# Kernel optimization log

Hardware: AMD Instinct MI355X
Metric: run time of the kernel (lower is better)

The kernel has to match this reference:

```python
import jax, jax.numpy as jnp
import numpy as np

B, T, D, H = 2048, 512, 32, 64


def _gru_layer(x, W_ih, W_hh, b_ih, b_hh):
    # x: [B, T, Din]; W_ih: [3H, Din]; W_hh: [3H, H]; gate order r, z, n (PyTorch).
    xp = jnp.einsum('btd,gd->btg', x, W_ih) + b_ih  # precompute input projections [B,T,3H]

    def step(h, xt):
        gh = h @ W_hh.T + b_hh                      # [B,3H]
        ir, iz, inn = jnp.split(xt, 3, axis=-1)
        hr, hz, hn = jnp.split(gh, 3, axis=-1)
        r = jax.nn.sigmoid(ir + hr)
        z = jax.nn.sigmoid(iz + hz)
        n = jnp.tanh(inn + r * hn)
        h_new = (1.0 - z) * n + z * h
        return h_new, h_new

    h0 = jnp.zeros((x.shape[0], W_hh.shape[1]), dtype=x.dtype)
    _, ys = jax.lax.scan(step, h0, xp.transpose(1, 0, 2))  # ys: [T,B,H]
    return ys.transpose(1, 0, 2)                           # [B,T,H]


def setup_inputs() -> dict:
    key = jax.random.key(0)
    ks = jax.random.split(key, 12)
    s_in = 1.0 / np.sqrt(H)
    u = lambda k, shp: jax.random.uniform(k, shp, jnp.float32, -s_in, s_in)
    return {
        'x': jax.random.normal(ks[0], (B, T, D), jnp.float32),
        'W_ih0': u(ks[1], (3 * H, D)),  'W_hh0': u(ks[2], (3 * H, H)),
        'b_ih0': u(ks[3], (3 * H,)),    'b_hh0': u(ks[4], (3 * H,)),
        'W_ih1': u(ks[5], (3 * H, H)),  'W_hh1': u(ks[6], (3 * H, H)),
        'b_ih1': u(ks[7], (3 * H,)),    'b_hh1': u(ks[8], (3 * H,)),
        'fc_w': u(ks[9], (1, H)),       'fc_b': u(ks[10], (1,)),
    }


def reference(x, W_ih0, W_hh0, b_ih0, b_hh0, W_ih1, W_hh1, b_ih1, b_hh1, fc_w, fc_b):
    # 2-layer GRU (eval mode: inter-layer dropout is identity) + linear head on last step.
    h1 = _gru_layer(x, W_ih0, W_hh0, b_ih0, b_hh0)   # [B,T,H]
    h2 = _gru_layer(h1, W_ih1, W_hh1, b_ih1, b_hh1)  # [B,T,H]
    out = h2[:, -1, :] @ fc_w.T + fc_b               # [B,1]
    return out[:, 0]                                  # [B]
```

## Files before the change

kernel.cpp:

```cpp
#include <hip/hip_runtime.h>

#define Bsz  2048
#define Tlen 512
#define Din  32
#define Hd   64
#define BT   16
#define HS   72
#define SLOT (BT * HS)
#define SPINB (1 << 14)

typedef _Float16 half8 __attribute__((ext_vector_type(8)));
typedef _Float16 half4 __attribute__((ext_vector_type(4)));
typedef float    f32x4 __attribute__((ext_vector_type(4)));

#define MFMA(a, b, c) __builtin_amdgcn_mfma_f32_16x16x32_f16((a), (b), (c), 0, 0, 0)

__device__ __forceinline__ half8 load8s(const float* p, float s) {
    half8 r;
#pragma unroll
    for (int j = 0; j < 8; ++j) r[j] = (_Float16)(p[j] * s);
    return r;
}
__device__ __forceinline__ half8 cvt8(float4 a, float4 b) {
    half8 r;
    r[0] = (_Float16)a.x; r[1] = (_Float16)a.y; r[2] = (_Float16)a.z; r[3] = (_Float16)a.w;
    r[4] = (_Float16)b.x; r[5] = (_Float16)b.y; r[6] = (_Float16)b.z; r[7] = (_Float16)b.w;
    return r;
}

__device__ __forceinline__ half4 gate_upd(const f32x4& gr, const f32x4& gz,
                                          const f32x4& anx, const f32x4& anh,
                                          float hst[4]) {
    half4 pk;
#pragma unroll
    for (int r = 0; r < 4; ++r) {
        float Er = __builtin_amdgcn_exp2f(gr[r]);
        float rr = __builtin_amdgcn_rcpf(1.0f + Er);
        float yy = anx[r] + rr * anh[r];
        float En = __builtin_amdgcn_exp2f(yy);
        float Ez = __builtin_amdgcn_exp2f(gz[r]);
        float num = Ez * (1.0f - En) + hst[r] * (1.0f + En);
        float den = (1.0f + Ez) * (1.0f + En);
        hst[r] = num * __builtin_amdgcn_rcpf(den);
        pk[r] = (_Float16)hst[r];
    }
    return pk;
}

#define SPIN_GE(CTR, TGT, CACHE)                                         \
  do {                                                                   \
    if ((CACHE) < (TGT)) {                                               \
      int v_ = (CACHE);                                                  \
      for (int sp_ = 0; v_ < (TGT) && sp_ < SPINB; ++sp_) {              \
        if (lane == 0)                                                   \
          v_ = __hip_atomic_load(&CTR, __ATOMIC_ACQUIRE,                 \
                                 __HIP_MEMORY_SCOPE_WORKGROUP);          \
        v_ = __builtin_amdgcn_readfirstlane(v_);                         \
        if (v_ < (TGT)) __builtin_amdgcn_s_sleep(1);                     \
      }                                                                  \
      (CACHE) = v_;                                                      \
    }                                                                    \
    __builtin_amdgcn_sched_barrier(0);                                   \
  } while (0)

__global__ __launch_bounds__(512, 2)
void gru_fused(const float* __restrict__ x,
               const float* __restrict__ Wih0, const float* __restrict__ Whh0,
               const float* __restrict__ bih0, const float* __restrict__ bhh0,
               const float* __restrict__ Wih1, const float* __restrict__ Whh1,
               const float* __restrict__ bih1, const float* __restrict__ bhh1,
               const float* __restrict__ fcw,  const float* __restrict__ fcb,
               float* __restrict__ out)
{
    __shared__ _Float16 h1r[4 * SLOT];
    __shared__ _Float16 h2r[2 * SLOT];
    __shared__ float hfin[BT][Hd];
    __shared__ int c1, c2, u1;

    const int tid  = threadIdx.x;
    const int lane = tid & 63;
    const int wave = tid >> 6;
    const int grp  = wave >> 2;
    const int wg   = wave & 3;
    const int m    = lane & 15;
    const int quad = lane >> 4;
    const int col  = (wg << 4) + m;
    const int gc   = (wg << 4) + (quad << 2);
    const int b0   = blockIdx.x << 4;

    for (int idx = tid; idx < SLOT; idx += 512) {
        h1r[3 * SLOT + idx] = (_Float16)0.f;
        h2r[SLOT + idx]     = (_Float16)0.f;
    }
    if (tid == 0) { c1 = 0; c2 = 0; u1 = 0; }

    const float sRZ = -1.44269504f;
    const float sN  = -2.88539008f;
    const int rdoff = m * HS + quad * 8;
    const int wroff = m * HS + gc;
    float hst[4] = {0.f, 0.f, 0.f, 0.f};

    __syncthreads();

    if (grp == 0) {
        half8 wx0, wx1, wx2, wh[2][3];
        f32x4 brz0v, brz1v, binv, bhnv;
        wx0 = load8s(Wih0 + (      col) * Din + quad * 8, sRZ);
        wx1 = load8s(Wih0 + ( 64 + col) * Din + quad * 8, sRZ);
        wx2 = load8s(Wih0 + (128 + col) * Din + quad * 8, sN);
#pragma unroll
        for (int kb = 0; kb < 2; ++kb) {
            wh[kb][0] = load8s(Whh0 + (      col) * Hd + kb * 32 + quad * 8, sRZ);
            wh[kb][1] = load8s(Whh0 + ( 64 + col) * Hd + kb * 32 + quad * 8, sRZ);
            wh[kb][2] = load8s(Whh0 + (128 + col) * Hd + kb * 32 + quad * 8, sN);
        }
#pragma unroll
        for (int r = 0; r < 4; ++r) {
            brz0v[r] = sRZ * (bih0[gc + r] + bhh0[gc + r]);
            brz1v[r] = sRZ * (bih0[64 + gc + r] + bhh0[64 + gc + r]);
            binv[r]  = sN * bih0[128 + gc + r];
            bhnv[r]  = sN * bhh0[128 + gc + r];
        }
        const float* xgp = x + (size_t)(b0 + m) * (Tlen * Din) + quad * 8;
        float4 x0a, x0b, x1a, x1b;
        x0a = *(const float4*)(xgp);        x0b = *(const float4*)(xgp + 4);
        x1a = *(const float4*)(xgp + Din);  x1b = *(const float4*)(xgp + Din + 4);
        int c1v = 0, u1v = 0;

#define STEP_A(T, xa_, xb_)                                              \
  do {                                                                   \
    SPIN_GE(c1, 4 * (T), c1v);                \
    const _Float16* s1 = h1r + (((T) + 3) & 3) * SLOT + rdoff;           \
    half8 bh0 = *(const half8*)s1;                                       \
    half8 bh1 = *(const half8*)(s1 + 32);                                \
    half8 ax = cvt8(xa_, xb_);                                           \
    { const int nx = ((T) + 2 < Tlen) ? (T) + 2 : Tlen - 1;              \
      const float* p = xgp + (size_t)nx * Din;                           \
      xa_ = *(const float4*)p; xb_ = *(const float4*)(p + 4); }          \
    f32x4 arx = brz0v, azx = brz1v, anx = binv;                          \
    f32x4 arh = {0.f,0.f,0.f,0.f}, azh = {0.f,0.f,0.f,0.f}, anh = bhnv;  \
    arh = MFMA(wh[0][0], bh0, arh); arh = MFMA(wh[1][0], bh1, arh);      \
    azh = MFMA(wh[0][1], bh0, azh); azh = MFMA(wh[1][1], bh1, azh);      \
    anh = MFMA(wh[0][2], bh0, anh); anh = MFMA(wh[1][2], bh1, anh);      \
    arx = MFMA(wx0, ax, arx);                                            \
    azx = MFMA(wx1, ax, azx);                                            \
    anx = MFMA(wx2, ax, anx);                                            \
    f32x4 gr = arx + arh, gz = azx + azh;                                \
    half4 pk = gate_upd(gr, gz, anx, anh, hst);                          \
    SPIN_GE(u1, 4 * ((T) - 3), u1v);          \
    *(half4*)(h1r + ((T) & 3) * SLOT + wroff) = pk;                      \
    asm volatile("s_waitcnt lgkmcnt(0)" ::: "memory");                   \
    if (lane == 0)                                                       \
      __hip_atomic_fetch_add(&c1, 1, __ATOMIC_RELEASE,                   \
                             __HIP_MEMORY_SCOPE_WORKGROUP);              \
  } while (0)

        for (int t = 0; t < Tlen; t += 2) {
            STEP_A(t,     x0a, x0b);
            STEP_A(t + 1, x1a, x1b);
        }
#undef STEP_A
    } else {
        half8 wx[2][3], wh[2][3];
        f32x4 brz0v, brz1v, binv, bhnv;
#pragma unroll
        for (int kb = 0; kb < 2; ++kb) {
            wx[kb][0] = load8s(Wih1 + (      col) * Hd + kb * 32 + quad * 8, sRZ);
            wx[kb][1] = load8s(Wih1 + ( 64 + col) * Hd + kb * 32 + quad * 8, sRZ);
            wx[kb][2] = load8s(Wih1 + (128 + col) * Hd + kb * 32 + quad * 8, sN);
            wh[kb][0] = load8s(Whh1 + (      col) * Hd + kb * 32 + quad * 8, sRZ);
            wh[kb][1] = load8s(Whh1 + ( 64 + col) * Hd + kb * 32 + quad * 8, sRZ);
            wh[kb][2] = load8s(Whh1 + (128 + col) * Hd + kb * 32 + quad * 8, sN);
        }
#pragma unroll
        for (int r = 0; r < 4; ++r) {
            brz0v[r] = sRZ * (bih1[gc + r] + bhh1[gc + r]);
            brz1v[r] = sRZ * (bih1[64 + gc + r] + bhh1[64 + gc + r]);
            binv[r]  = sN * bih1[128 + gc + r];
            bhnv[r]  = sN * bhh1[128 + gc + r];
        }
        int c1v = 0, c2v = 0;

#define STEP_B(T)                                                        \
  do {                                                                   \
    SPIN_GE(c2, 4 * (T), c2v);                \
    SPIN_GE(c1, 4 * ((T) + 1), c1v);          \
    const _Float16* s1 = h1r + ((T) & 3) * SLOT + rdoff;    \
    const _Float16* s2 = h2r + (((T) + 1) & 1) * SLOT + rdoff;  \
    half8 bx0 = *(const half8*)s1;                                       \
    half8 bx1 = *(const half8*)(s1 + 32);                                \
    half8 bh0 = *(const half8*)s2;                                       \
    half8 bh1 = *(const half8*)(s2 + 32);                                \
    f32x4 arx = brz0v, azx = brz1v, anx = binv;                          \
    f32x4 arh = {0.f,0.f,0.f,0.f}, azh = {0.f,0.f,0.f,0.f}, anh = bhnv;  \
    arx = MFMA(wx[0][0], bx0, arx); arx = MFMA(wx[1][0], bx1, arx);      \
    azx = MFMA(wx[0][1], bx0, azx); azx = MFMA(wx[1][1], bx1, azx);      \
    anx = MFMA(wx[0][2], bx0, anx); anx = MFMA(wx[1][2], bx1, anx);      \
    arh = MFMA(wh[0][0], bh0, arh); arh = MFMA(wh[1][0], bh1, arh);      \
    azh = MFMA(wh[0][1], bh0, azh); azh = MFMA(wh[1][1], bh1, azh);      \
    anh = MFMA(wh[0][2], bh0, anh); anh = MFMA(wh[1][2], bh1, anh);      \
    asm volatile("s_waitcnt lgkmcnt(0)" ::: "memory");   \
    if (lane == 0)                                                       \
      __hip_atomic_fetch_add(&u1, 1, __ATOMIC_RELEASE,                   \
                             __HIP_MEMORY_SCOPE_WORKGROUP);              \
    f32x4 gr = arx + arh, gz = azx + azh;                                \
    half4 pk = gate_upd(gr, gz, anx, anh, hst);                          \
    *(half4*)(h2r + ((T) & 1) * SLOT + wroff) = pk;                      \
    if ((T) == Tlen - 1) {                                               \
      f32x4 fv;                                                          \
      for (int r = 0; r < 4; ++r) fv[r] = hst[r];                        \
      *(f32x4*)(&hfin[m][gc]) = fv;                                      \
    }                                                                    \
    asm volatile("s_waitcnt lgkmcnt(0)" ::: "memory");                   \
    if (lane == 0)                                                       \
      __hip_atomic_fetch_add(&c2, 1, __ATOMIC_RELEASE,                   \
                             __HIP_MEMORY_SCOPE_WORKGROUP);              \
  } while (0)

        for (int t = 0; t < Tlen; t += 2) {
            STEP_B(t);
            STEP_B(t + 1);
        }
#undef STEP_B

        if (wg == 0) {
            SPIN_GE(c2, 4 * Tlen, c2v);
            if (lane < BT) {
                float acc = fcb[0];
                for (int c = 0; c < Hd; ++c) acc += hfin[lane][c] * fcw[c];
                out[b0 + lane] = acc;
            }
        }
    }
}

extern "C" void kernel_launch(void* const* d_in, const int* in_sizes, int n_in,
                              void* d_out, int out_size, void* d_ws, size_t ws_size,
                              hipStream_t stream) {
    gru_fused<<<dim3(Bsz / BT), dim3(512), 0, stream>>>(
        (const float*)d_in[0],
        (const float*)d_in[1], (const float*)d_in[2],
        (const float*)d_in[3], (const float*)d_in[4],
        (const float*)d_in[5], (const float*)d_in[6],
        (const float*)d_in[7], (const float*)d_in[8],
        (const float*)d_in[9], (const float*)d_in[10],
        (float*)d_out);
}
```

Baseline: 535.8 us.

## Replace LDS spin-counter sync with lockstep barrier regions between GRU layers

Removes the atomic counter spin-wait protocol between the layer-0 and layer-1 wave groups. Both groups now advance in lockstep regions separated by s_barrier, with layer 1 running one step behind layer 0. Layer 0's input projection for the next step is computed in the second half of each region so it overlaps the layer-1 gate update. This trades spin-polling and sleep latency for two full-workgroup barriers per step, drops the 2-blocks-per-CU launch bound, and uses a larger LDS arena.

```diff
diff --git a/kernel.cpp b/kernel.cpp
--- a/kernel.cpp
+++ b/kernel.cpp
@@ -6,14 +6,19 @@
 #define Hd   64
 #define BT   16
 #define HS   72
-#define SLOT (BT * HS)
-#define SPINB (1 << 14)
+#define BUFE 2048
 
 typedef _Float16 half8 __attribute__((ext_vector_type(8)));
 typedef _Float16 half4 __attribute__((ext_vector_type(4)));
 typedef float    f32x4 __attribute__((ext_vector_type(4)));
 
 #define MFMA(a, b, c) __builtin_amdgcn_mfma_f32_16x16x32_f16((a), (b), (c), 0, 0, 0)
+
+#define BARRIER()                                              \
+  do {                                                         \
+    asm volatile("s_waitcnt lgkmcnt(0)" ::: "memory");         \
+    __builtin_amdgcn_s_barrier();                              \
+  } while (0)
 
 __device__ __forceinline__ half8 load8s(const float* p, float s) {
     half8 r;
@@ -47,23 +52,7 @@
     return pk;
 }
 
-#define SPIN_GE(CTR, TGT, CACHE)                                         \
-  do {                                                                   \
-    if ((CACHE) < (TGT)) {                                               \
-      int v_ = (CACHE);                                                  \
-      for (int sp_ = 0; v_ < (TGT) && sp_ < SPINB; ++sp_) {              \
-        if (lane == 0)                                                   \
-          v_ = __hip_atomic_load(&CTR, __ATOMIC_ACQUIRE,                 \
-                                 __HIP_MEMORY_SCOPE_WORKGROUP);          \
-        v_ = __builtin_amdgcn_readfirstlane(v_);                         \
-        if (v_ < (TGT)) __builtin_amdgcn_s_sleep(1);                     \
-      }                                                                  \
-      (CACHE) = v_;                                                      \
-    }                                                                    \
-    __builtin_amdgcn_sched_barrier(0);                                   \
-  } while (0)
-
-__global__ __launch_bounds__(512, 2)
+__global__ __launch_bounds__(512)
 void gru_fused(const float* __restrict__ x,
                const float* __restrict__ Wih0, const float* __restrict__ Whh0,
                const float* __restrict__ bih0, const float* __restrict__ bhh0,
@@ -72,10 +61,8 @@
                const float* __restrict__ fcw,  const float* __restrict__ fcb,
                float* __restrict__ out)
 {
-    __shared__ _Float16 h1r[4 * SLOT];
-    __shared__ _Float16 h2r[2 * SLOT];
+    __shared__ _Float16 arena[4 * BUFE];
     __shared__ float hfin[BT][Hd];
-    __shared__ int c1, c2, u1;
 
     const int tid  = threadIdx.x;
     const int lane = tid & 63;
@@ -88,11 +75,7 @@
     const int gc   = (wg << 4) + (quad << 2);
     const int b0   = blockIdx.x << 4;
 
-    for (int idx = tid; idx < SLOT; idx += 512) {
-        h1r[3 * SLOT + idx] = (_Float16)0.f;
-        h2r[SLOT + idx]     = (_Float16)0.f;
-    }
-    if (tid == 0) { c1 = 0; c2 = 0; u1 = 0; }
+    for (int idx = tid; idx < 4 * BUFE; idx += 512) arena[idx] = (_Float16)0.f;
 
     const float sRZ = -1.44269504f;
     const float sN  = -2.88539008f;
@@ -100,14 +83,12 @@
     const int wroff = m * HS + gc;
     float hst[4] = {0.f, 0.f, 0.f, 0.f};
 
-    __syncthreads();
-
+    half8 wx[2][3], wh[2][3];
+    f32x4 brz0v, brz1v, binv, bhnv;
     if (grp == 0) {
-        half8 wx0, wx1, wx2, wh[2][3];
-        f32x4 brz0v, brz1v, binv, bhnv;
-        wx0 = load8s(Wih0 + (      col) * Din + quad * 8, sRZ);
-        wx1 = load8s(Wih0 + ( 64 + col) * Din + quad * 8, sRZ);
-        wx2 = load8s(Wih0 + (128 + col) * Din + quad * 8, sN);
+        wx[0][0] = load8s(Wih0 + (      col) * Din + quad * 8, sRZ);
+        wx[0][1] = load8s(Wih0 + ( 64 + col) * Din + quad * 8, sRZ);
+        wx[0][2] = load8s(Wih0 + (128 + col) * Din + quad * 8, sN);
 #pragma unroll
         for (int kb = 0; kb < 2; ++kb) {
             wh[kb][0] = load8s(Whh0 + (      col) * Hd + kb * 32 + quad * 8, sRZ);
@@ -121,48 +102,7 @@
             binv[r]  = sN * bih0[128 + gc + r];
             bhnv[r]  = sN * bhh0[128 + gc + r];
         }
-        const float* xgp = x + (size_t)(b0 + m) * (Tlen * Din) + quad * 8;
-        float4 x0a, x0b, x1a, x1b;
-        x0a = *(const float4*)(xgp);        x0b = *(const float4*)(xgp + 4);
-        x1a = *(const float4*)(xgp + Din);  x1b = *(const float4*)(xgp + Din + 4);
-        int c1v = 0, u1v = 0;
-
-#define STEP_A(T, xa_, xb_)                                              \
-  do {                                                                   \
-    SPIN_GE(c1, 4 * (T), c1v);                \
-    const _Float16* s1 = h1r + (((T) + 3) & 3) * SLOT + rdoff;           \
-    half8 bh0 = *(const half8*)s1;                                       \
-    half8 bh1 = *(const half8*)(s1 + 32);                                \
-    half8 ax = cvt8(xa_, xb_);                                           \
-    { const int nx = ((T) + 2 < Tlen) ? (T) + 2 : Tlen - 1;              \
-      const float* p = xgp + (size_t)nx * Din;                           \
-      xa_ = *(const float4*)p; xb_ = *(const float4*)(p + 4); }          \
-    f32x4 arx = brz0v, azx = brz1v, anx = binv;                          \
-    f32x4 arh = {0.f,0.f,0.f,0.f}, azh = {0.f,0.f,0.f,0.f}, anh = bhnv;  \
-    arh = MFMA(wh[0][0], bh0, arh); arh = MFMA(wh[1][0], bh1, arh);      \
-    azh = MFMA(wh[0][1], bh0, azh); azh = MFMA(wh[1][1], bh1, azh);      \
-    anh = MFMA(wh[0][2], bh0, anh); anh = MFMA(wh[1][2], bh1, anh);      \
-    arx = MFMA(wx0, ax, arx);                                            \
-    azx = MFMA(wx1, ax, azx);                                            \
-    anx = MFMA(wx2, ax, anx);                                            \
-    f32x4 gr = arx + arh, gz = azx + azh;                                \
-    half4 pk = gate_upd(gr, gz, anx, anh, hst);                          \
-    SPIN_GE(u1, 4 * ((T) - 3), u1v);          \
-    *(half4*)(h1r + ((T) & 3) * SLOT + wroff) = pk;                      \
-    asm volatile("s_waitcnt lgkmcnt(0)" ::: "memory");                   \
-    if (lane == 0)                                                       \
-      __hip_atomic_fetch_add(&c1, 1, __ATOMIC_RELEASE,                   \
-                             __HIP_MEMORY_SCOPE_WORKGROUP);              \
-  } while (0)
-
-        for (int t = 0; t < Tlen; t += 2) {
-            STEP_A(t,     x0a, x0b);
-            STEP_A(t + 1, x1a, x1b);
-        }
-#undef STEP_A
     } else {
-        half8 wx[2][3], wh[2][3];
-        f32x4 brz0v, brz1v, binv, bhnv;
 #pragma unroll
         for (int kb = 0; kb < 2; ++kb) {
             wx[kb][0] = load8s(Wih1 + (      col) * Hd + kb * 32 + quad * 8, sRZ);
@@ -179,58 +119,112 @@
             binv[r]  = sN * bih1[128 + gc + r];
             bhnv[r]  = sN * bhh1[128 + gc + r];
         }
-        int c1v = 0, c2v = 0;
-
-#define STEP_B(T)                                                        \
+    }
+
+    const float* xgp = x + (size_t)(b0 + m) * (Tlen * Din) + quad * 8;
+    float4 x0a, x0b, x1a, x1b;
+    f32x4 xar, xaz, xan;
+    if (grp == 0) {
+        x0a = *(const float4*)(xgp);        x0b = *(const float4*)(xgp + 4);
+        x1a = *(const float4*)(xgp + Din);  x1b = *(const float4*)(xgp + Din + 4);
+        half8 ax = cvt8(x0a, x0b);
+        xar = brz0v; xar = MFMA(wx[0][0], ax, xar);
+        xaz = brz1v; xaz = MFMA(wx[0][1], ax, xaz);
+        xan = binv;  xan = MFMA(wx[0][2], ax, xan);
+        {
+            const float* p = xgp + 2 * Din;
+            x0a = *(const float4*)p; x0b = *(const float4*)(p + 4);
+        }
+    }
+    half8 bx0, bx1;
+    f32x4 arx, azx, anx, arh, azh, anh;
+
+    __syncthreads();
+
+#define REGION(I, RO, WO, XA, XB, DO1)                                   \
   do {                                                                   \
-    SPIN_GE(c2, 4 * (T), c2v);                \
-    SPIN_GE(c1, 4 * ((T) + 1), c1v);          \
-    const _Float16* s1 = h1r + ((T) & 3) * SLOT + rdoff;    \
-    const _Float16* s2 = h2r + (((T) + 1) & 1) * SLOT + rdoff;  \
-    half8 bx0 = *(const half8*)s1;                                       \
-    half8 bx1 = *(const half8*)(s1 + 32);                                \
-    half8 bh0 = *(const half8*)s2;                                       \
-    half8 bh1 = *(const half8*)(s2 + 32);                                \
-    f32x4 arx = brz0v, azx = brz1v, anx = binv;                          \
-    f32x4 arh = {0.f,0.f,0.f,0.f}, azh = {0.f,0.f,0.f,0.f}, anh = bhnv;  \
-    arx = MFMA(wx[0][0], bx0, arx); arx = MFMA(wx[1][0], bx1, arx);      \
-    azx = MFMA(wx[0][1], bx0, azx); azx = MFMA(wx[1][1], bx1, azx);      \
-    anx = MFMA(wx[0][2], bx0, anx); anx = MFMA(wx[1][2], bx1, anx);      \
-    arh = MFMA(wh[0][0], bh0, arh); arh = MFMA(wh[1][0], bh1, arh);      \
-    azh = MFMA(wh[0][1], bh0, azh); azh = MFMA(wh[1][1], bh1, azh);      \
-    anh = MFMA(wh[0][2], bh0, anh); anh = MFMA(wh[1][2], bh1, anh);      \
-    asm volatile("s_waitcnt lgkmcnt(0)" ::: "memory");   \
-    if (lane == 0)                                                       \
-      __hip_atomic_fetch_add(&u1, 1, __ATOMIC_RELEASE,                   \
-                             __HIP_MEMORY_SCOPE_WORKGROUP);              \
-    f32x4 gr = arx + arh, gz = azx + azh;                                \
-    half4 pk = gate_upd(gr, gz, anx, anh, hst);                          \
-    *(half4*)(h2r + ((T) & 1) * SLOT + wroff) = pk;                      \
-    if ((T) == Tlen - 1) {                                               \
-      f32x4 fv;                                                          \
-      for (int r = 0; r < 4; ++r) fv[r] = hst[r];                        \
-      *(f32x4*)(&hfin[m][gc]) = fv;                                      \
+                             \
+    if (grp == 0) {                                                      \
+      const _Float16* s1 = arena + (RO) + rdoff;                         \
+      half8 bh0 = *(const half8*)s1;                                     \
+      half8 bh1 = *(const half8*)(s1 + 32);                              \
+      f32x4 arh0 = {0.f,0.f,0.f,0.f}, azh0 = {0.f,0.f,0.f,0.f};          \
+      f32x4 anh0 = bhnv;                                                 \
+      arh0 = MFMA(wh[0][0], bh0, arh0); arh0 = MFMA(wh[1][0], bh1, arh0);\
+      azh0 = MFMA(wh[0][1], bh0, azh0); azh0 = MFMA(wh[1][1], bh1, azh0);\
+      anh0 = MFMA(wh[0][2], bh0, anh0); anh0 = MFMA(wh[1][2], bh1, anh0);\
+      f32x4 gr = xar + arh0, gz = xaz + azh0;                            \
+      half4 pk = gate_upd(gr, gz, xan, anh0, hst);                       \
+      *(half4*)(arena + (WO) + wroff) = pk;                              \
+    } else if (DO1) {                                                    \
+      const _Float16* s2 = arena + 2 * BUFE + (RO) + rdoff;              \
+      half8 bh0 = *(const half8*)s2;                                     \
+      half8 bh1 = *(const half8*)(s2 + 32);                              \
+      arx = brz0v; azx = brz1v; anx = binv;                              \
+      arh = (f32x4){0.f,0.f,0.f,0.f}; azh = (f32x4){0.f,0.f,0.f,0.f};    \
+      anh = bhnv;                                                        \
+      arx = MFMA(wx[0][0], bx0, arx); arx = MFMA(wx[1][0], bx1, arx);    \
+      azx = MFMA(wx[0][1], bx0, azx); azx = MFMA(wx[1][1], bx1, azx);    \
+      anx = MFMA(wx[0][2], bx0, anx); anx = MFMA(wx[1][2], bx1, anx);    \
+      arh = MFMA(wh[0][0], bh0, arh); arh = MFMA(wh[1][0], bh1, arh);    \
+      azh = MFMA(wh[0][1], bh0, azh); azh = MFMA(wh[1][1], bh1, azh);    \
+      anh = MFMA(wh[0][2], bh0, anh); anh = MFMA(wh[1][2], bh1, anh);    \
     }                                                                    \
-    asm volatile("s_waitcnt lgkmcnt(0)" ::: "memory");                   \
-    if (lane == 0)                                                       \
-      __hip_atomic_fetch_add(&c2, 1, __ATOMIC_RELEASE,                   \
-                             __HIP_MEMORY_SCOPE_WORKGROUP);              \
+    BARRIER();                                                           \
+                             \
+    if (grp == 0) {                                                      \
+      half8 ax = cvt8(XA, XB);                               \
+      { const int nx = ((I) + 3 < Tlen) ? (I) + 3 : Tlen - 1;            \
+        const float* p = xgp + (size_t)nx * Din;                         \
+        XA = *(const float4*)p; XB = *(const float4*)(p + 4); }          \
+      xar = brz0v; xar = MFMA(wx[0][0], ax, xar);                        \
+      xaz = brz1v; xaz = MFMA(wx[0][1], ax, xaz);                        \
+      xan = binv;  xan = MFMA(wx[0][2], ax, xan);                        \
+    } else {                                                             \
+      if (DO1) {                                                         \
+        f32x4 gr = arx + arh, gz = azx + azh;                            \
+        half4 pk = gate_upd(gr, gz, anx, anh, hst);                      \
+        *(half4*)(arena + 2 * BUFE + (WO) + wroff) = pk;                 \
+      }                                                                  \
+      const _Float16* s1n = arena + (WO) + rdoff;     \
+      bx0 = *(const half8*)s1n;                                          \
+      bx1 = *(const half8*)(s1n + 32);                                   \
+    }                                                                    \
+    BARRIER();                                                           \
   } while (0)
 
-        for (int t = 0; t < Tlen; t += 2) {
-            STEP_B(t);
-            STEP_B(t + 1);
-        }
-#undef STEP_B
-
-        if (wg == 0) {
-            SPIN_GE(c2, 4 * Tlen, c2v);
-            if (lane < BT) {
-                float acc = fcb[0];
-                for (int c = 0; c < Hd; ++c) acc += hfin[lane][c] * fcw[c];
-                out[b0 + lane] = acc;
-            }
-        }
+    REGION(0, BUFE, 0, x1a, x1b, 0);
+    for (int i = 1; i + 1 < Tlen; i += 2) {
+        REGION(i,     0,    BUFE, x0a, x0b, 1);
+        REGION(i + 1, BUFE, 0,    x1a, x1b, 1);
+    }
+    REGION(Tlen - 1, 0, BUFE, x0a, x0b, 1);
+#undef REGION
+
+    if (grp == 1) {
+        const _Float16* s2 = arena + 2 * BUFE + BUFE + rdoff;
+        half8 bh0 = *(const half8*)s2;
+        half8 bh1 = *(const half8*)(s2 + 32);
+        f32x4 arx2 = brz0v, azx2 = brz1v, anx2 = binv;
+        f32x4 arh2 = {0.f,0.f,0.f,0.f}, azh2 = {0.f,0.f,0.f,0.f}, anh2 = bhnv;
+        arx2 = MFMA(wx[0][0], bx0, arx2); arx2 = MFMA(wx[1][0], bx1, arx2);
+        azx2 = MFMA(wx[0][1], bx0, azx2); azx2 = MFMA(wx[1][1], bx1, azx2);
+        anx2 = MFMA(wx[0][2], bx0, anx2); anx2 = MFMA(wx[1][2], bx1, anx2);
+        arh2 = MFMA(wh[0][0], bh0, arh2); arh2 = MFMA(wh[1][0], bh1, arh2);
+        azh2 = MFMA(wh[0][1], bh0, azh2); azh2 = MFMA(wh[1][1], bh1, azh2);
+        anh2 = MFMA(wh[0][2], bh0, anh2); anh2 = MFMA(wh[1][2], bh1, anh2);
+        f32x4 gr = arx2 + arh2, gz = azx2 + azh2;
+        gate_upd(gr, gz, anx2, anh2, hst);
+        f32x4 fv;
+#pragma unroll
+        for (int r = 0; r < 4; ++r) fv[r] = hst[r];
+        *(f32x4*)(&hfin[m][gc]) = fv;
+    }
+    __syncthreads();
+    if (tid < BT) {
+        float acc = fcb[0];
+        for (int c = 0; c < Hd; ++c) acc += hfin[tid][c] * fcw[c];
+        out[b0 + tid] = acc;
     }
 }
 
```

New measurement: 487.6 us. -9.0%, faster.

## Collapse each GRU layer to a single wave with deeper inter-layer ring

Applied to the files above, without the earlier changes.

Each layer's recurrence is now computed by one wave covering all 64 hidden columns, where before four waves each handled 16 columns. This removes intra-layer cross-wave synchronisation on every timestep. The layer-1 to layer-2 buffer grows to an 8-slot ring so layer 1 can run further ahead, and the FC head becomes a register dot product with shuffles. The trade-off is 4x more serial MFMA and gate work per wave per step, much higher register pressure from holding all weights, and only 128 threads per block.

```diff
diff --git a/kernel.cpp b/kernel.cpp
--- a/kernel.cpp
+++ b/kernel.cpp
@@ -7,7 +7,8 @@
 #define BT   16
 #define HS   72
 #define SLOT (BT * HS)
-#define SPINB (1 << 14)
+#define RS   8
+#define SPINB 4096
 
 typedef _Float16 half8 __attribute__((ext_vector_type(8)));
 typedef _Float16 half4 __attribute__((ext_vector_type(4)));
@@ -28,9 +29,9 @@
     return r;
 }
 
-__device__ __forceinline__ half4 gate_upd(const f32x4& gr, const f32x4& gz,
-                                          const f32x4& anx, const f32x4& anh,
-                                          float hst[4]) {
+__device__ __forceinline__ half4 gate4(const f32x4& gr, const f32x4& gz,
+                                       const f32x4& anx, const f32x4& anh,
+                                       float* hst) {
     half4 pk;
 #pragma unroll
     for (int r = 0; r < 4; ++r) {
@@ -63,181 +64,192 @@
     __builtin_amdgcn_sched_barrier(0);                                   \
   } while (0)
 
-__global__ __launch_bounds__(512, 2)
-void gru_fused(const float* __restrict__ x,
-               const float* __restrict__ Wih0, const float* __restrict__ Whh0,
-               const float* __restrict__ bih0, const float* __restrict__ bhh0,
-               const float* __restrict__ Wih1, const float* __restrict__ Whh1,
-               const float* __restrict__ bih1, const float* __restrict__ bhh1,
-               const float* __restrict__ fcw,  const float* __restrict__ fcb,
-               float* __restrict__ out)
+__global__ __launch_bounds__(128, 1)
+void gru_ws(const float* __restrict__ x,
+            const float* __restrict__ Wih0, const float* __restrict__ Whh0,
+            const float* __restrict__ bih0, const float* __restrict__ bhh0,
+            const float* __restrict__ Wih1, const float* __restrict__ Whh1,
+            const float* __restrict__ bih1, const float* __restrict__ bhh1,
+            const float* __restrict__ fcw,  const float* __restrict__ fcb,
+            float* __restrict__ out)
 {
-    __shared__ _Float16 h1r[4 * SLOT];
+    __shared__ _Float16 ring[RS * SLOT];
     __shared__ _Float16 h2r[2 * SLOT];
-    __shared__ float hfin[BT][Hd];
-    __shared__ int c1, c2, u1;
+    __shared__ int c1, u1;
 
     const int tid  = threadIdx.x;
     const int lane = tid & 63;
-    const int wave = tid >> 6;
-    const int grp  = wave >> 2;
-    const int wg   = wave & 3;
+    const int wv   = tid >> 6;
+    const int q    = lane >> 4;
     const int m    = lane & 15;
-    const int quad = lane >> 4;
-    const int col  = (wg << 4) + m;
-    const int gc   = (wg << 4) + (quad << 2);
     const int b0   = blockIdx.x << 4;
 
-    for (int idx = tid; idx < SLOT; idx += 512) {
-        h1r[3 * SLOT + idx] = (_Float16)0.f;
-        h2r[SLOT + idx]     = (_Float16)0.f;
+    for (int idx = tid; idx < SLOT; idx += 128) {
+        ring[(RS - 1) * SLOT + idx] = (_Float16)0.f;
+        h2r[SLOT + idx]             = (_Float16)0.f;
     }
-    if (tid == 0) { c1 = 0; c2 = 0; u1 = 0; }
+    if (tid == 0) { c1 = 0; u1 = 0; }
 
     const float sRZ = -1.44269504f;
     const float sN  = -2.88539008f;
-    const int rdoff = m * HS + quad * 8;
-    const int wroff = m * HS + gc;
-    float hst[4] = {0.f, 0.f, 0.f, 0.f};
+    const int rd = m * HS + q * 8;
+    const int wr = m * HS + q * 4;
+    float hst[16];
+#pragma unroll
+    for (int i = 0; i < 16; ++i) hst[i] = 0.f;
 
     __syncthreads();
 
-    if (grp == 0) {
-        half8 wx0, wx1, wx2, wh[2][3];
-        f32x4 brz0v, brz1v, binv, bhnv;
-        wx0 = load8s(Wih0 + (      col) * Din + quad * 8, sRZ);
-        wx1 = load8s(Wih0 + ( 64 + col) * Din + quad * 8, sRZ);
-        wx2 = load8s(Wih0 + (128 + col) * Din + quad * 8, sN);
-#pragma unroll
-        for (int kb = 0; kb < 2; ++kb) {
-            wh[kb][0] = load8s(Whh0 + (      col) * Hd + kb * 32 + quad * 8, sRZ);
-            wh[kb][1] = load8s(Whh0 + ( 64 + col) * Hd + kb * 32 + quad * 8, sRZ);
-            wh[kb][2] = load8s(Whh0 + (128 + col) * Hd + kb * 32 + quad * 8, sN);
+    if (wv == 0) {
+        half8 wxr[4], wxz[4], wxn[4];
+        half8 whr[4][2], whz[4][2], whn[4][2];
+        f32x4 br[4], bz[4], bnx[4], bnh[4];
+#pragma unroll
+        for (int g = 0; g < 4; ++g) {
+            wxr[g] = load8s(Wih0 + (      16 * g + m) * Din + q * 8, sRZ);
+            wxz[g] = load8s(Wih0 + ( 64 + 16 * g + m) * Din + q * 8, sRZ);
+            wxn[g] = load8s(Wih0 + (128 + 16 * g + m) * Din + q * 8, sN);
+#pragma unroll
+            for (int kf = 0; kf < 2; ++kf) {
+                whr[g][kf] = load8s(Whh0 + (      16*g + m) * Hd + kf*32 + q*8, sRZ);
+                whz[g][kf] = load8s(Whh0 + ( 64 + 16*g + m) * Hd + kf*32 + q*8, sRZ);
+                whn[g][kf] = load8s(Whh0 + (128 + 16*g + m) * Hd + kf*32 + q*8, sN);
+            }
+#pragma unroll
+            for (int u = 0; u < 4; ++u) {
+                const int c = 16 * g + 4 * q + u;
+                br[g][u]  = sRZ * (bih0[c] + bhh0[c]);
+                bz[g][u]  = sRZ * (bih0[64 + c] + bhh0[64 + c]);
+                bnx[g][u] = sN * bih0[128 + c];
+                bnh[g][u] = sN * bhh0[128 + c];
+            }
         }
-#pragma unroll
-        for (int r = 0; r < 4; ++r) {
-            brz0v[r] = sRZ * (bih0[gc + r] + bhh0[gc + r]);
-            brz1v[r] = sRZ * (bih0[64 + gc + r] + bhh0[64 + gc + r]);
-            binv[r]  = sN * bih0[128 + gc + r];
-            bhnv[r]  = sN * bhh0[128 + gc + r];
+        const float* xgp = x + (size_t)(b0 + m) * (Tlen * Din) + q * 8;
+        float4 x0a = *(const float4*)(xgp),       x0b = *(const float4*)(xgp + 4);
+        float4 x1a = *(const float4*)(xgp + Din), x1b = *(const float4*)(xgp + Din + 4);
+        int u1v = 0;
+
+        auto l1step = [&](int T, float4& XA, float4& XB) {
+            if (T >= RS) SPIN_GE(u1, T - (RS - 1), u1v);
+            half8 ax = cvt8(XA, XB);
+            { const int nx = (T + 2 < Tlen) ? T + 2 : Tlen - 1;
+              const float* p = xgp + (size_t)nx * Din;
+              XA = *(const float4*)p; XB = *(const float4*)(p + 4); }
+            const _Float16* s1 = ring + ((T + RS - 1) & (RS - 1)) * SLOT + rd;
+            half8 bh0 = *(const half8*)s1;
+            half8 bh1 = *(const half8*)(s1 + 32);
+            f32x4 gr4[4], gz4[4], gnx[4], gnh[4];
+#pragma unroll
+            for (int g = 0; g < 4; ++g) {
+                f32x4 arx = MFMA(wxr[g], ax, br[g]);
+                f32x4 arh = {0.f, 0.f, 0.f, 0.f};
+                arh = MFMA(whr[g][0], bh0, arh); arh = MFMA(whr[g][1], bh1, arh);
+                f32x4 azx = MFMA(wxz[g], ax, bz[g]);
+                f32x4 azh = {0.f, 0.f, 0.f, 0.f};
+                azh = MFMA(whz[g][0], bh0, azh); azh = MFMA(whz[g][1], bh1, azh);
+                gnx[g] = MFMA(wxn[g], ax, bnx[g]);
+                f32x4 anh = bnh[g];
+                anh = MFMA(whn[g][0], bh0, anh); anh = MFMA(whn[g][1], bh1, anh);
+                gnh[g] = anh;
+                gr4[g] = arx + arh; gz4[g] = azx + azh;
+            }
+            _Float16* wp = ring + (T & (RS - 1)) * SLOT + wr;
+#pragma unroll
+            for (int g = 0; g < 4; ++g) {
+                half4 pk = gate4(gr4[g], gz4[g], gnx[g], gnh[g], &hst[4 * g]);
+                *(half4*)(wp + 16 * g) = pk;
+            }
+            asm volatile("s_waitcnt lgkmcnt(0)" ::: "memory");
+            if (lane == 0)
+                __hip_atomic_fetch_add(&c1, 1, __ATOMIC_RELEASE,
+                                       __HIP_MEMORY_SCOPE_WORKGROUP);
+        };
+        for (int t = 0; t < Tlen; t += 2) {
+            l1step(t,     x0a, x0b);
+            l1step(t + 1, x1a, x1b);
         }
-        const float* xgp = x + (size_t)(b0 + m) * (Tlen * Din) + quad * 8;
-        float4 x0a, x0b, x1a, x1b;
-        x0a = *(const float4*)(xgp);        x0b = *(const float4*)(xgp + 4);
-        x1a = *(const float4*)(xgp + Din);  x1b = *(const float4*)(xgp + Din + 4);
-        int c1v = 0, u1v = 0;
-
-#define STEP_A(T, xa_, xb_)                                              \
-  do {                                                                   \
-    SPIN_GE(c1, 4 * (T), c1v);                \
-    const _Float16* s1 = h1r + (((T) + 3) & 3) * SLOT + rdoff;           \
-    half8 bh0 = *(const half8*)s1;                                       \
-    half8 bh1 = *(const half8*)(s1 + 32);                                \
-    half8 ax = cvt8(xa_, xb_);                                           \
-    { const int nx = ((T) + 2 < Tlen) ? (T) + 2 : Tlen - 1;              \
-      const float* p = xgp + (size_t)nx * Din;                           \
-      xa_ = *(const float4*)p; xb_ = *(const float4*)(p + 4); }          \
-    f32x4 arx = brz0v, azx = brz1v, anx = binv;                          \
-    f32x4 arh = {0.f,0.f,0.f,0.f}, azh = {0.f,0.f,0.f,0.f}, anh = bhnv;  \
-    arh = MFMA(wh[0][0], bh0, arh); arh = MFMA(wh[1][0], bh1, arh);      \
-    azh = MFMA(wh[0][1], bh0, azh); azh = MFMA(wh[1][1], bh1, azh);      \
-    anh = MFMA(wh[0][2], bh0, anh); anh = MFMA(wh[1][2], bh1, anh);      \
-    arx = MFMA(wx0, ax, arx);                                            \
-    azx = MFMA(wx1, ax, azx);                                            \
-    anx = MFMA(wx2, ax, anx);                                            \
-    f32x4 gr = arx + arh, gz = azx + azh;                                \
-    half4 pk = gate_upd(gr, gz, anx, anh, hst);                          \
-    SPIN_GE(u1, 4 * ((T) - 3), u1v);          \
-    *(half4*)(h1r + ((T) & 3) * SLOT + wroff) = pk;                      \
-    asm volatile("s_waitcnt lgkmcnt(0)" ::: "memory");                   \
-    if (lane == 0)                                                       \
-      __hip_atomic_fetch_add(&c1, 1, __ATOMIC_RELEASE,                   \
-                             __HIP_MEMORY_SCOPE_WORKGROUP);              \
-  } while (0)
-
-        for (int t = 0; t < Tlen; t += 2) {
-            STEP_A(t,     x0a, x0b);
-            STEP_A(t + 1, x1a, x1b);
+    } else {
+        half8 wir[4][2], wiz[4][2], win[4][2];
+        half8 whr[4][2], whz[4][2], whn[4][2];
+        f32x4 br[4], bz[4], bnx[4], bnh[4];
+        float fcv[16];
+#pragma unroll
+        for (int g = 0; g < 4; ++g) {
+#pragma unroll
+            for (int kf = 0; kf < 2; ++kf) {
+                wir[g][kf] = load8s(Wih1 + (      16*g + m) * Hd + kf*32 + q*8, sRZ);
+                wiz[g][kf] = load8s(Wih1 + ( 64 + 16*g + m) * Hd + kf*32 + q*8, sRZ);
+                win[g][kf] = load8s(Wih1 + (128 + 16*g + m) * Hd + kf*32 + q*8, sN);
+                whr[g][kf] = load8s(Whh1 + (      16*g + m) * Hd + kf*32 + q*8, sRZ);
+                whz[g][kf] = load8s(Whh1 + ( 64 + 16*g + m) * Hd + kf*32 + q*8, sRZ);
+                whn[g][kf] = load8s(Whh1 + (128 + 16*g + m) * Hd + kf*32 + q*8, sN);
+            }
+#pragma unroll
+            for (int u = 0; u < 4; ++u) {
+                const int c = 16 * g + 4 * q + u;
+                br[g][u]  = sRZ * (bih1[c] + bhh1[c]);
+                bz[g][u]  = sRZ * (bih1[64 + c] + bhh1[64 + c]);
+                bnx[g][u] = sN * bih1[128 + c];
+                bnh[g][u] = sN * bhh1[128 + c];
+                fcv[4 * g + u] = fcw[c];
+            }
         }
-#undef STEP_A
-    } else {
-        half8 wx[2][3], wh[2][3];
-        f32x4 brz0v, brz1v, binv, bhnv;
-#pragma unroll
-        for (int kb = 0; kb < 2; ++kb) {
-            wx[kb][0] = load8s(Wih1 + (      col) * Hd + kb * 32 + quad * 8, sRZ);
-            wx[kb][1] = load8s(Wih1 + ( 64 + col) * Hd + kb * 32 + quad * 8, sRZ);
-            wx[kb][2] = load8s(Wih1 + (128 + col) * Hd + kb * 32 + quad * 8, sN);
-            wh[kb][0] = load8s(Whh1 + (      col) * Hd + kb * 32 + quad * 8, sRZ);
-            wh[kb][1] = load8s(Whh1 + ( 64 + col) * Hd + kb * 32 + quad * 8, sRZ);
-            wh[kb][2] = load8s(Whh1 + (128 + col) * Hd + kb * 32 + quad * 8, sN);
-        }
-#pragma unroll
-        for (int r = 0; r < 4; ++r) {
-            brz0v[r] = sRZ * (bih1[gc + r] + bhh1[gc + r]);
-            brz1v[r] = sRZ * (bih1[64 + gc + r] + bhh1[64 + gc + r]);
-            binv[r]  = sN * bih1[128 + gc + r];
-            bhnv[r]  = sN * bhh1[128 + gc + r];
-        }
-        int c1v = 0, c2v = 0;
-
-#define STEP_B(T)                                                        \
-  do {                                                                   \
-    SPIN_GE(c2, 4 * (T), c2v);                \
-    SPIN_GE(c1, 4 * ((T) + 1), c1v);          \
-    const _Float16* s1 = h1r + ((T) & 3) * SLOT + rdoff;    \
-    const _Float16* s2 = h2r + (((T) + 1) & 1) * SLOT + rdoff;  \
-    half8 bx0 = *(const half8*)s1;                                       \
-    half8 bx1 = *(const half8*)(s1 + 32);                                \
-    half8 bh0 = *(const half8*)s2;                                       \
-    half8 bh1 = *(const half8*)(s2 + 32);                                \
-    f32x4 arx = brz0v, azx = brz1v, anx = binv;                          \
-    f32x4 arh = {0.f,0.f,0.f,0.f}, azh = {0.f,0.f,0.f,0.f}, anh = bhnv;  \
-    arx = MFMA(wx[0][0], bx0, arx); arx = MFMA(wx[1][0], bx1, arx);      \
-    azx = MFMA(wx[0][1], bx0, azx); azx = MFMA(wx[1][1], bx1, azx);      \
-    anx = MFMA(wx[0][2], bx0, anx); anx = MFMA(wx[1][2], bx1, anx);      \
-    arh = MFMA(wh[0][0], bh0, arh); arh = MFMA(wh[1][0], bh1, arh);      \
-    azh = MFMA(wh[0][1], bh0, azh); azh = MFMA(wh[1][1], bh1, azh);      \
-    anh = MFMA(wh[0][2], bh0, anh); anh = MFMA(wh[1][2], bh1, anh);      \
-    asm volatile("s_waitcnt lgkmcnt(0)" ::: "memory");   \
-    if (lane == 0)                                                       \
-      __hip_atomic_fetch_add(&u1, 1, __ATOMIC_RELEASE,                   \
-                             __HIP_MEMORY_SCOPE_WORKGROUP);              \
-    f32x4 gr = arx + arh, gz = azx + azh;                                \
-    half4 pk = gate_upd(gr, gz, anx, anh, hst);                          \
-    *(half4*)(h2r + ((T) & 1) * SLOT + wroff) = pk;                      \
-    if ((T) == Tlen - 1) {                                               \
-      f32x4 fv;                                                          \
-      for (int r = 0; r < 4; ++r) fv[r] = hst[r];                        \
-      *(f32x4*)(&hfin[m][gc]) = fv;                                      \
-    }                                                                    \
-    asm volatile("s_waitcnt lgkmcnt(0)" ::: "memory");                   \
-    if (lane == 0)                                                       \
-      __hip_atomic_fetch_add(&c2, 1, __ATOMIC_RELEASE,                   \
-                             __HIP_MEMORY_SCOPE_WORKGROUP);              \
-  } while (0)
-
-        for (int t = 0; t < Tlen; t += 2) {
-            STEP_B(t);
-            STEP_B(t + 1);
-        }
-#undef STEP_B
-
-        if (wg == 0) {
-            SPIN_GE(c2, 4 * Tlen, c2v);
-            if (lane < BT) {
-                float acc = fcb[0];
-                for (int c = 0; c < Hd; ++c) acc += hfin[lane][c] * fcw[c];
-                out[b0 + lane] = acc;
-            }
-        }
+        int c1v = 0;
+
+        auto l2step = [&](int T) {
+            SPIN_GE(c1, T + 1, c1v);
+            const _Float16* s1 = ring + (T & (RS - 1)) * SLOT + rd;
+            half8 bx0 = *(const half8*)s1;
+            half8 bx1 = *(const half8*)(s1 + 32);
+            const _Float16* s2 = h2r + ((T + 1) & 1) * SLOT + rd;
+            half8 bh0 = *(const half8*)s2;
+            half8 bh1 = *(const half8*)(s2 + 32);
+            asm volatile("s_waitcnt lgkmcnt(0)" ::: "memory");
+            __builtin_amdgcn_sched_barrier(0);
+            if (lane == 0)
+                __hip_atomic_fetch_add(&u1, 1, __ATOMIC_RELEASE,
+                                       __HIP_MEMORY_SCOPE_WORKGROUP);
+            f32x4 gr4[4], gz4[4], gnx[4], gnh[4];
+#pragma unroll
+            for (int g = 0; g < 4; ++g) {
+                f32x4 arx = MFMA(wir[g][0], bx0, br[g]);
+                arx = MFMA(wir[g][1], bx1, arx);
+                f32x4 arh = {0.f, 0.f, 0.f, 0.f};
+                arh = MFMA(whr[g][0], bh0, arh); arh = MFMA(whr[g][1], bh1, arh);
+                f32x4 azx = MFMA(wiz[g][0], bx0, bz[g]);
+                azx = MFMA(wiz[g][1], bx1, azx);
+                f32x4 azh = {0.f, 0.f, 0.f, 0.f};
+                azh = MFMA(whz[g][0], bh0, azh); azh = MFMA(whz[g][1], bh1, azh);
+                f32x4 anx = MFMA(win[g][0], bx0, bnx[g]);
+                anx = MFMA(win[g][1], bx1, anx);
+                gnx[g] = anx;
+                f32x4 anh = bnh[g];
+                anh = MFMA(whn[g][0], bh0, anh); anh = MFMA(whn[g][1], bh1, anh);
+                gnh[g] = anh;
+                gr4[g] = arx + arh; gz4[g] = azx + azh;
+            }
+            _Float16* wp = h2r + (T & 1) * SLOT + wr;
+#pragma unroll
+            for (int g = 0; g < 4; ++g) {
+                half4 pk = gate4(gr4[g], gz4[g], gnx[g], gnh[g], &hst[4 * g]);
+                *(half4*)(wp + 16 * g) = pk;
+            }
+        };
+        for (int t = 0; t < Tlen; ++t) l2step(t);
+
+        float acc = 0.f;
+#pragma unroll
+        for (int i = 0; i < 16; ++i) acc += hst[i] * fcv[i];
+        acc += __shfl_xor(acc, 16);
+        acc += __shfl_xor(acc, 32);
+        if (lane < 16) out[b0 + m] = acc + fcb[0];
     }
 }
 
 extern "C" void kernel_launch(void* const* d_in, const int* in_sizes, int n_in,
                               void* d_out, int out_size, void* d_ws, size_t ws_size,
                               hipStream_t stream) {
-    gru_fused<<<dim3(Bsz / BT), dim3(512), 0, stream>>>(
+    gru_ws<<<dim3(Bsz / BT), dim3(128), 0, stream>>>(
         (const float*)d_in[0],
         (const float*)d_in[1], (const float*)d_in[2],
         (const float*)d_in[3], (const float*)d_in[4],
```

Measured after the change: 759.9 us. 1.42x slower.
